# Performance work log

Hardware: AMD Instinct MI355X
Metric: run time of the kernel (lower is better)

Reference implementation:

```python
import jax, jax.numpy as jnp
import numpy as np

N, H, F, E, K = 2048, 1024, 4096, 8, 2


def setup_inputs() -> dict:
    key = jax.random.key(0)
    ks = jax.random.split(key, 6)
    x = jax.random.normal(ks[0], (N, H), dtype=jnp.float32)
    mapping = jax.random.randint(ks[1], (N, K), 0, E)
    Wg = jax.random.normal(ks[2], (E, H), dtype=jnp.float32) * (1.0 / np.sqrt(H))
    W1 = jax.random.normal(ks[3], (E, H, F), dtype=jnp.float32) * (1.0 / np.sqrt(H))
    b1 = jnp.zeros((E, F), dtype=jnp.float32)
    W2 = jax.random.normal(ks[4], (E, F, H), dtype=jnp.float32) * (1.0 / np.sqrt(F))
    b2 = jnp.zeros((E, H), dtype=jnp.float32)
    return {"x": x, "mapping": mapping, "Wg": Wg, "W1": W1, "b1": b1, "W2": W2, "b2": b2}


def reference(x, mapping, Wg, W1, b1, W2, b2):
    # Gate logits: note original applies softmax over dim=0 (the token axis).
    logits = jax.nn.softmax(x @ Wg.T, axis=0)  # [N, E]

    # Per-expert MLP. Original sorts tokens by expert, runs per-expert GEMMs on
    # dynamic splits, then unsorts -- mathematically: y[i,k] = MLP_{mapping[i,k]}(x[i]).
    # JIT-friendly dense baseline: run every expert over all tokens, gather per token.
    def mlp(e):
        h = jax.nn.gelu(x @ W1[e] + b1[e])  # [N, F]
        return h @ W2[e] + b2[e]            # [N, H]

    y_all = jnp.stack([mlp(e) for e in range(E)])  # [E, N, H]

    # Gate weights gathered per (token, k), normalized over top-k.
    w = jnp.take_along_axis(logits, mapping, axis=1)  # [N, K]
    w = w / jnp.sum(w, axis=-1, keepdims=True)

    idx = jnp.arange(x.shape[0])
    out = jnp.zeros_like(x)
    for k in range(mapping.shape[1]):
        yk = y_all[mapping[:, k], idx]  # [N, H] gather per token's k-th expert
        out = out + yk * w[:, k:k + 1]
    return out
```

## Files before the change

kernel.cpp:

```cpp
#include <hip/hip_runtime.h>

#define N_TOK 2048
#define HD    1024
#define FD    4096
#define NE    8

typedef __attribute__((ext_vector_type(8))) short short8;
typedef __attribute__((ext_vector_type(4))) float floatx4;

__device__ __forceinline__ unsigned short f2bf(float f) {
  unsigned int u = __float_as_uint(f);
  u += 0x7fffu + ((u >> 16) & 1u);
  return (unsigned short)(u >> 16);
}

__device__ __forceinline__ void gl2lds16(const unsigned short* g, unsigned short* l) {
  __builtin_amdgcn_global_load_lds(
      (const __attribute__((address_space(1))) unsigned int*)g,
      (__attribute__((address_space(3))) unsigned int*)l, 16, 0, 0);
}

__device__ __forceinline__ float gelu_tanh(float x) {
  float t = 0.7978845608028654f * x * (1.0f + 0.044715f * x * x);
  return 0.5f * x * (1.0f + tanhf(t));
}

__device__ __forceinline__ int poff_of(const int* __restrict__ cnt, int e) {
  int o = 0;
  for (int i = 0; i < e; ++i) o += (cnt[i] + 127) & ~127;
  return o;
}

__global__ void k_gating(const float* __restrict__ x, const float* __restrict__ wg,
                         float* __restrict__ p) {
  int wave = threadIdx.x >> 6;
  int lane = threadIdx.x & 63;
  int n = blockIdx.x * 4 + wave;
  const float4* xr = (const float4*)(x + (size_t)n * HD);
  float4 xv[4];
  #pragma unroll
  for (int i = 0; i < 4; ++i) xv[i] = xr[lane + i * 64];
  for (int e = 0; e < NE; ++e) {
    const float4* wr = (const float4*)(wg + (size_t)e * HD);
    float s = 0.f;
    #pragma unroll
    for (int i = 0; i < 4; ++i) {
      float4 w4 = wr[lane + i * 64];
      s += xv[i].x * w4.x + xv[i].y * w4.y + xv[i].z * w4.z + xv[i].w * w4.w;
    }
    for (int o = 32; o > 0; o >>= 1) s += __shfl_xor(s, o, 64);
    if (lane == 0) p[e * N_TOK + n] = s;
  }
}

__global__ void k_softmax(float* __restrict__ p) {
  int e = blockIdx.x;
  float* col = p + e * N_TOK;
  __shared__ float red[256];
  int t = threadIdx.x;
  float m = -1e30f;
  for (int i = t; i < N_TOK; i += 256) m = fmaxf(m, col[i]);
  red[t] = m; __syncthreads();
  for (int s = 128; s > 0; s >>= 1) { if (t < s) red[t] = fmaxf(red[t], red[t + s]); __syncthreads(); }
  m = red[0]; __syncthreads();
  float sum = 0.f;
  for (int i = t; i < N_TOK; i += 256) { float v = expf(col[i] - m); col[i] = v; sum += v; }
  red[t] = sum; __syncthreads();
  for (int s = 128; s > 0; s >>= 1) { if (t < s) red[t] += red[t + s]; __syncthreads(); }
  float inv = 1.0f / red[0];
  for (int i = t; i < N_TOK; i += 256) col[i] *= inv;
}

__global__ void k_route(const int* __restrict__ mp, const float* __restrict__ p,
                        int* __restrict__ cnt, int* __restrict__ idxl,
                        int* __restrict__ tke, int* __restrict__ tks, float* __restrict__ tkw) {
  int n = blockIdx.x * 256 + threadIdx.x;
  if (n >= N_TOK) return;
  int m0 = mp[n * 2 + 0], m1 = mp[n * 2 + 1];
  if (m0 == m1) {
    int s = atomicAdd(&cnt[m0], 1);
    idxl[m0 * N_TOK + s] = n;
    tke[n * 2] = m0; tks[n * 2] = s; tkw[n * 2] = 1.0f;
    tke[n * 2 + 1] = m0; tks[n * 2 + 1] = s; tkw[n * 2 + 1] = 0.0f;
  } else {
    float p0 = p[m0 * N_TOK + n], p1 = p[m1 * N_TOK + n];
    float inv = 1.0f / (p0 + p1);
    int s0 = atomicAdd(&cnt[m0], 1);
    idxl[m0 * N_TOK + s0] = n;
    tke[n * 2] = m0; tks[n * 2] = s0; tkw[n * 2] = p0 * inv;
    int s1 = atomicAdd(&cnt[m1], 1);
    idxl[m1 * N_TOK + s1] = n;
    tke[n * 2 + 1] = m1; tks[n * 2 + 1] = s1; tkw[n * 2 + 1] = p1 * inv;
  }
}

__global__ void k_gather(const float* __restrict__ x, const int* __restrict__ cnt,
                         const int* __restrict__ idxl, unsigned short* __restrict__ xg) {
  int e = blockIdx.y;
  int r = blockIdx.x;
  int c = cnt[e];
  int pc = (c + 127) & ~127;
  if (r >= pc) return;
  unsigned short* dst = xg + ((size_t)poff_of(cnt, e) + r) * HD;
  int t = threadIdx.x;
  union { unsigned short us[8]; uint4 v; } o;
  if (r < c) {
    const float* src = x + (size_t)idxl[e * N_TOK + r] * HD;
    float4 f0 = ((const float4*)src)[t * 2];
    float4 f1 = ((const float4*)src)[t * 2 + 1];
    o.us[0] = f2bf(f0.x); o.us[1] = f2bf(f0.y); o.us[2] = f2bf(f0.z); o.us[3] = f2bf(f0.w);
    o.us[4] = f2bf(f1.x); o.us[5] = f2bf(f1.y); o.us[6] = f2bf(f1.z); o.us[7] = f2bf(f1.w);
  } else {
    o.v.x = 0u; o.v.y = 0u; o.v.z = 0u; o.v.w = 0u;
  }
  ((uint4*)dst)[t] = o.v;
}

__global__ __launch_bounds__(256) void k_transcvt2(const float* __restrict__ w1,
                                                   unsigned short* __restrict__ w1t,
                                                   const float* __restrict__ w2,
                                                   unsigned short* __restrict__ w2t) {
  __shared__ float tile[64][65];
  int l = blockIdx.x;
  const float* src; unsigned short* dst; int rows, cols, bx, by, e;
  if (l < 8192) {
    src = w1; dst = w1t; rows = HD; cols = FD;
    bx = l & 63; by = (l >> 6) & 15; e = l >> 10;
  } else {
    int l2 = l - 8192;
    src = w2; dst = w2t; rows = FD; cols = HD;
    bx = l2 & 15; by = (l2 >> 4) & 63; e = l2 >> 10;
  }
  const size_t base = (size_t)e * rows * cols;
  int c0 = bx * 64, r0 = by * 64;
  int t = threadIdx.x;
  int lr = t >> 4;
  int lc = (t & 15) * 4;
  #pragma unroll
  for (int i = 0; i < 64; i += 16) {
    float4 v = *(const float4*)(src + base + (size_t)(r0 + lr + i) * cols + c0 + lc);
    tile[lr + i][lc] = v.x; tile[lr + i][lc + 1] = v.y;
    tile[lr + i][lc + 2] = v.z; tile[lr + i][lc + 3] = v.w;
  }
  __syncthreads();
  int oc = t >> 2;
  int rseg = (t & 3) * 16;
  union { unsigned short us[16]; uint4 v[2]; } o;
  #pragma unroll
  for (int i = 0; i < 16; ++i) o.us[i] = f2bf(tile[rseg + i][oc]);
  unsigned short* d = dst + base + (size_t)(c0 + oc) * rows + r0 + rseg;
  ((uint4*)d)[0] = o.v[0];
  ((uint4*)d)[1] = o.v[1];
}

__global__ __launch_bounds__(256) void k_gemm1(
    const unsigned short* __restrict__ xg, const unsigned short* __restrict__ w1t,
    const float* __restrict__ b1, const int* __restrict__ cnt,
    unsigned short* __restrict__ h) {
  const int l = blockIdx.x;
  const int r = l & 7;
  const int m = (l >> 3) & 31;
  const int q = l >> 8;
  const int e = q >> 2;
  const int n = ((q & 3) << 3) | r;

  const int c = cnt[e];
  const int mbase = m * 64;
  if (mbase >= c) return;
  const int nbase = n * 128;
  const int po = poff_of(cnt, e);
  const unsigned short* A = xg + ((size_t)po + mbase) * HD;
  const unsigned short* B = w1t + ((size_t)e * FD + nbase) * HD;

  __shared__ unsigned short As[64 * 32];
  __shared__ unsigned short Bs[128 * 32];

  const int tid = threadIdx.x;
  const int wave = tid >> 6, lane = tid & 63;
  const int quad = lane >> 4, lrow = lane & 15;
  const int wn = wave * 32;

  floatx4 acc[4][2];
  #pragma unroll
  for (int i = 0; i < 4; ++i)
    #pragma unroll
    for (int j = 0; j < 2; ++j) acc[i][j] = (floatx4){0.f, 0.f, 0.f, 0.f};

  const int rA = tid >> 2, kA = (((tid & 3) ^ ((tid >> 2) & 3)) & 3) * 8;
  const int rB0 = tid >> 2, kB0 = kA;
  const int rB1 = 64 + (tid >> 2), kB1 = kA;

  const int sx = lrow & 3;

  for (int kt = 0; kt < HD / 32; ++kt) {
    __syncthreads();
    const unsigned short* ga = A + kt * 32;
    const unsigned short* gb = B + kt * 32;
    gl2lds16(ga + (size_t)rA * HD + kA, As + (size_t)(wave * 64) * 8);
    gl2lds16(gb + (size_t)rB0 * HD + kB0, Bs + (size_t)(wave * 64) * 8);
    gl2lds16(gb + (size_t)rB1 * HD + kB1, Bs + (size_t)(256 + wave * 64) * 8);
    __syncthreads();
    short8 aF[4], bF[2];
    #pragma unroll
    for (int i = 0; i < 4; ++i)
      aF[i] = *(const short8*)(As + (i * 16 + lrow) * 32 + ((quad ^ sx) & 3) * 8);
    #pragma unroll
    for (int j = 0; j < 2; ++j)
      bF[j] = *(const short8*)(Bs + (wn + j * 16 + lrow) * 32 + ((quad ^ sx) & 3) * 8);
    #pragma unroll
    for (int i = 0; i < 4; ++i)
      #pragma unroll
      for (int j = 0; j < 2; ++j)
        acc[i][j] = __builtin_amdgcn_mfma_f32_16x16x32_bf16(aF[i], bF[j], acc[i][j], 0, 0, 0);
  }

  const size_t hrow0 = (size_t)po + mbase;
  #pragma unroll
  for (int i = 0; i < 4; ++i) {
    #pragma unroll
    for (int rr = 0; rr < 4; ++rr) {
      int row = i * 16 + quad * 4 + rr;
      unsigned short* hr = h + (hrow0 + row) * FD + nbase;
      #pragma unroll
      for (int j = 0; j < 2; ++j) {
        int col = wn + j * 16 + lrow;
        float v = acc[i][j][rr] + b1[e * FD + nbase + col];
        hr[col] = f2bf(gelu_tanh(v));
      }
    }
  }
}

__global__ __launch_bounds__(256) void k_gemm2(
    const unsigned short* __restrict__ h, const unsigned short* __restrict__ w2t,
    const int* __restrict__ cnt, unsigned short* __restrict__ ya) {
  const int l = blockIdx.x;
  const int nt = l & 15;
  const int mt = l >> 4;
  const int mbase = mt * 64;
  const int nbase = nt * 64;

  int e = -1, po = 0, ce = 0;
  {
    int o = 0;
    #pragma unroll
    for (int i = 0; i < NE; ++i) {
      int ci = cnt[i];
      int pc = (ci + 127) & ~127;
      if (mbase >= o && mbase < o + pc) { e = i; po = o; ce = ci; }
      o += pc;
    }
  }
  if (e < 0) return;
  if (mbase - po >= ce) return;

  const unsigned short* A = h + (size_t)mbase * FD;
  const unsigned short* B = w2t + ((size_t)e * HD + nbase) * FD;

  __shared__ unsigned short As[64 * 64];
  __shared__ unsigned short Bs[64 * 64];

  const int tid = threadIdx.x;
  const int wave = tid >> 6, lane = tid & 63;
  const int quad = lane >> 4, lrow = lane & 15;
  const int wm = (wave >> 1) * 32, wn = (wave & 1) * 32;

  floatx4 acc[2][2];
  #pragma unroll
  for (int i = 0; i < 2; ++i)
    #pragma unroll
    for (int j = 0; j < 2; ++j) acc[i][j] = (floatx4){0.f, 0.f, 0.f, 0.f};

  const int s0 = tid,       r0 = s0 >> 3, k0 = (((s0 & 7) ^ ((s0 >> 3) & 7)) & 7) * 8;
  const int s1 = 256 + tid, r1 = s1 >> 3, k1 = (((s1 & 7) ^ ((s1 >> 3) & 7)) & 7) * 8;

  const int sx8 = lrow & 7;

  for (int kt = 0; kt < FD / 64; ++kt) {
    __syncthreads();
    const unsigned short* ga = A + kt * 64;
    const unsigned short* gb = B + kt * 64;
    gl2lds16(ga + (size_t)r0 * FD + k0, As + (size_t)(wave * 64) * 8);
    gl2lds16(ga + (size_t)r1 * FD + k1, As + (size_t)(256 + wave * 64) * 8);
    gl2lds16(gb + (size_t)r0 * FD + k0, Bs + (size_t)(wave * 64) * 8);
    gl2lds16(gb + (size_t)r1 * FD + k1, Bs + (size_t)(256 + wave * 64) * 8);
    __syncthreads();
    #pragma unroll
    for (int c = 0; c < 2; ++c) {
      short8 aF[2], bF[2];
      #pragma unroll
      for (int i = 0; i < 2; ++i)
        aF[i] = *(const short8*)(As + (wm + i * 16 + lrow) * 64 + (((c * 4 + quad) ^ sx8) & 7) * 8);
      #pragma unroll
      for (int j = 0; j < 2; ++j)
        bF[j] = *(const short8*)(Bs + (wn + j * 16 + lrow) * 64 + (((c * 4 + quad) ^ sx8) & 7) * 8);
      #pragma unroll
      for (int i = 0; i < 2; ++i)
        #pragma unroll
        for (int j = 0; j < 2; ++j)
          acc[i][j] = __builtin_amdgcn_mfma_f32_16x16x32_bf16(aF[i], bF[j], acc[i][j], 0, 0, 0);
    }
  }

  #pragma unroll
  for (int i = 0; i < 2; ++i) {
    #pragma unroll
    for (int rr = 0; rr < 4; ++rr) {
      int row = mbase + wm + i * 16 + quad * 4 + rr;
      unsigned short* yr = ya + (size_t)row * HD + nbase;
      #pragma unroll
      for (int j = 0; j < 2; ++j) {
        int col = wn + j * 16 + lrow;
        yr[col] = f2bf(acc[i][j][rr]);
      }
    }
  }
}

__global__ __launch_bounds__(256) void k_combine(
    const unsigned short* __restrict__ ya, const float* __restrict__ b2,
    const int* __restrict__ cnt, const int* __restrict__ tke,
    const int* __restrict__ tks, const float* __restrict__ tkw,
    float* __restrict__ out) {
  int n = blockIdx.x;
  int e0 = tke[n * 2], e1 = tke[n * 2 + 1];
  int p0 = poff_of(cnt, e0) + tks[n * 2];
  int p1 = poff_of(cnt, e1) + tks[n * 2 + 1];
  float w0 = tkw[n * 2], w1 = tkw[n * 2 + 1];
  int c = threadIdx.x * 4;
  union { unsigned short us[4]; ushort2 u2[2]; unsigned long long ll; } y0, y1;
  y0.ll = *(const unsigned long long*)(ya + (size_t)p0 * HD + c);
  y1.ll = *(const unsigned long long*)(ya + (size_t)p1 * HD + c);
  float4 bb0 = *(const float4*)(b2 + (size_t)e0 * HD + c);
  float4 bb1 = *(const float4*)(b2 + (size_t)e1 * HD + c);
  float4 o;
  o.x = w0 * (__uint_as_float((unsigned)y0.us[0] << 16) + bb0.x) + w1 * (__uint_as_float((unsigned)y1.us[0] << 16) + bb1.x);
  o.y = w0 * (__uint_as_float((unsigned)y0.us[1] << 16) + bb0.y) + w1 * (__uint_as_float((unsigned)y1.us[1] << 16) + bb1.y);
  o.z = w0 * (__uint_as_float((unsigned)y0.us[2] << 16) + bb0.z) + w1 * (__uint_as_float((unsigned)y1.us[2] << 16) + bb1.z);
  o.w = w0 * (__uint_as_float((unsigned)y0.us[3] << 16) + bb0.w) + w1 * (__uint_as_float((unsigned)y1.us[3] << 16) + bb1.w);
  *(float4*)(out + (size_t)n * HD + c) = o;
}

extern "C" void kernel_launch(void* const* d_in, const int* in_sizes, int n_in,
                              void* d_out, int out_size, void* d_ws, size_t ws_size,
                              hipStream_t stream) {
  const float* x  = (const float*)d_in[0];
  const int*   mp = (const int*)d_in[1];
  const float* wg = (const float*)d_in[2];
  const float* w1 = (const float*)d_in[3];
  const float* b1 = (const float*)d_in[4];
  const float* w2 = (const float*)d_in[5];
  const float* b2 = (const float*)d_in[6];
  float* out = (float*)d_out;
  char* ws = (char*)d_ws;

  float* p    = (float*)(ws + 0);
  int*   cnt  = (int*)(ws + 65536);
  int*   idxl = (int*)(ws + 66048);
  int*   tke  = (int*)(ws + 131584);
  int*   tks  = (int*)(ws + 147968);
  float* tkw  = (float*)(ws + 164352);
  size_t off = 180736;
  unsigned short* w1t = (unsigned short*)(ws + off);  off += 67108864;
  unsigned short* w2t = (unsigned short*)(ws + off);  off += 67108864;
  unsigned short* xg  = (unsigned short*)(ws + off);  off += 10485760;
  unsigned short* h   = (unsigned short*)(ws + off);  off += 41943040;
  unsigned short* ya  = (unsigned short*)(ws + off);  off += 10485760;

  hipMemsetAsync(cnt, 0, 32, stream);

  k_gating<<<512, 256, 0, stream>>>(x, wg, p);
  k_softmax<<<NE, 256, 0, stream>>>(p);
  k_route<<<NE, 256, 0, stream>>>(mp, p, cnt, idxl, tke, tks, tkw);
  k_transcvt2<<<16384, 256, 0, stream>>>(w1, w1t, w2, w2t);
  k_gather<<<dim3(N_TOK, NE), 128, 0, stream>>>(x, cnt, idxl, xg);
  k_gemm1<<<8192, 256, 0, stream>>>(xg, w1t, b1, cnt, h);
  k_gemm2<<<80 * 16, 256, 0, stream>>>(h, w2t, cnt, ya);
  k_combine<<<N_TOK, 256, 0, stream>>>(ya, b2, cnt, tke, tks, tkw, out);
}
```

Before: 494.3 us.

## Pre-tile converted expert weights into contiguous 128x32 blocks for GEMM loads

```diff
diff --git a/kernel.cpp b/kernel.cpp
--- a/kernel.cpp
+++ b/kernel.cpp
@@ -116,41 +116,44 @@
   ((uint4*)dst)[t] = o.v;
 }
 
-__global__ __launch_bounds__(256) void k_transcvt2(const float* __restrict__ w1,
+__global__ __launch_bounds__(256) void k_transtile(const float* __restrict__ w1,
                                                    unsigned short* __restrict__ w1t,
                                                    const float* __restrict__ w2,
                                                    unsigned short* __restrict__ w2t) {
-  __shared__ float tile[64][65];
+  __shared__ float tile[32][129];
   int l = blockIdx.x;
-  const float* src; unsigned short* dst; int rows, cols, bx, by, e;
+  const float* src; unsigned short* dst; int ncols; size_t tbase;
+  int e, nt, kt;
   if (l < 8192) {
-    src = w1; dst = w1t; rows = HD; cols = FD;
-    bx = l & 63; by = (l >> 6) & 15; e = l >> 10;
+    e = l >> 10; nt = (l >> 5) & 31; kt = l & 31;
+    src = w1 + (size_t)e * HD * FD; ncols = FD;
+    dst = w1t; tbase = (((size_t)e * 32 + nt) * 32 + kt) * 4096;
   } else {
     int l2 = l - 8192;
-    src = w2; dst = w2t; rows = FD; cols = HD;
-    bx = l2 & 15; by = (l2 >> 4) & 63; e = l2 >> 10;
-  }
-  const size_t base = (size_t)e * rows * cols;
-  int c0 = bx * 64, r0 = by * 64;
-  int t = threadIdx.x;
-  int lr = t >> 4;
-  int lc = (t & 15) * 4;
-  #pragma unroll
-  for (int i = 0; i < 64; i += 16) {
-    float4 v = *(const float4*)(src + base + (size_t)(r0 + lr + i) * cols + c0 + lc);
-    tile[lr + i][lc] = v.x; tile[lr + i][lc + 1] = v.y;
-    tile[lr + i][lc + 2] = v.z; tile[lr + i][lc + 3] = v.w;
+    e = l2 >> 10; nt = (l2 >> 7) & 7; kt = l2 & 127;
+    src = w2 + (size_t)e * FD * HD; ncols = HD;
+    dst = w2t; tbase = (((size_t)e * 8 + nt) * 128 + kt) * 4096;
+  }
+  const int t = threadIdx.x;
+  const int c4 = t & 31;
+  const int rb = t >> 5;
+  #pragma unroll
+  for (int i = 0; i < 4; ++i) {
+    int r = rb + 8 * i;
+    float4 v = *(const float4*)(src + (size_t)(kt * 32 + r) * ncols + nt * 128 + c4 * 4);
+    tile[r][c4 * 4 + 0] = v.x; tile[r][c4 * 4 + 1] = v.y;
+    tile[r][c4 * 4 + 2] = v.z; tile[r][c4 * 4 + 3] = v.w;
   }
   __syncthreads();
-  int oc = t >> 2;
-  int rseg = (t & 3) * 16;
-  union { unsigned short us[16]; uint4 v[2]; } o;
-  #pragma unroll
-  for (int i = 0; i < 16; ++i) o.us[i] = f2bf(tile[rseg + i][oc]);
-  unsigned short* d = dst + base + (size_t)(c0 + oc) * rows + r0 + rseg;
-  ((uint4*)d)[0] = o.v[0];
-  ((uint4*)d)[1] = o.v[1];
+  #pragma unroll
+  for (int i = 0; i < 2; ++i) {
+    int o = t * 2 + i;
+    int n = o >> 2, kc = o & 3;
+    union { unsigned short us[8]; uint4 v; } u;
+    #pragma unroll
+    for (int j = 0; j < 8; ++j) u.us[j] = f2bf(tile[kc * 8 + j][n]);
+    *(uint4*)(dst + tbase + (size_t)o * 8) = u.v;
+  }
 }
 
 __global__ __launch_bounds__(256) void k_gemm1(
@@ -170,7 +173,7 @@
   const int nbase = n * 128;
   const int po = poff_of(cnt, e);
   const unsigned short* A = xg + ((size_t)po + mbase) * HD;
-  const unsigned short* B = w1t + ((size_t)e * FD + nbase) * HD;
+  const unsigned short* Bt = w1t + (((size_t)e * 32 + n) * 32) * 4096;
 
   __shared__ unsigned short As[64 * 32];
   __shared__ unsigned short Bs[128 * 32];
@@ -186,27 +189,22 @@
     #pragma unroll
     for (int j = 0; j < 2; ++j) acc[i][j] = (floatx4){0.f, 0.f, 0.f, 0.f};
 
-  const int rA = tid >> 2, kA = (((tid & 3) ^ ((tid >> 2) & 3)) & 3) * 8;
-  const int rB0 = tid >> 2, kB0 = kA;
-  const int rB1 = 64 + (tid >> 2), kB1 = kA;
-
-  const int sx = lrow & 3;
+  const int rA = tid >> 2, kA = (tid & 3) * 8;
 
   for (int kt = 0; kt < HD / 32; ++kt) {
     __syncthreads();
-    const unsigned short* ga = A + kt * 32;
-    const unsigned short* gb = B + kt * 32;
-    gl2lds16(ga + (size_t)rA * HD + kA, As + (size_t)(wave * 64) * 8);
-    gl2lds16(gb + (size_t)rB0 * HD + kB0, Bs + (size_t)(wave * 64) * 8);
-    gl2lds16(gb + (size_t)rB1 * HD + kB1, Bs + (size_t)(256 + wave * 64) * 8);
+    gl2lds16(A + kt * 32 + (size_t)rA * HD + kA, As + (size_t)wave * 512);
+    const unsigned short* gb = Bt + (size_t)kt * 4096 + (size_t)tid * 8;
+    gl2lds16(gb,        Bs + (size_t)wave * 512);
+    gl2lds16(gb + 2048, Bs + 2048 + (size_t)wave * 512);
     __syncthreads();
     short8 aF[4], bF[2];
     #pragma unroll
     for (int i = 0; i < 4; ++i)
-      aF[i] = *(const short8*)(As + (i * 16 + lrow) * 32 + ((quad ^ sx) & 3) * 8);
+      aF[i] = *(const short8*)(As + (i * 16 + lrow) * 32 + quad * 8);
     #pragma unroll
     for (int j = 0; j < 2; ++j)
-      bF[j] = *(const short8*)(Bs + (wn + j * 16 + lrow) * 32 + ((quad ^ sx) & 3) * 8);
+      bF[j] = *(const short8*)(Bs + (wn + j * 16 + lrow) * 32 + quad * 8);
     #pragma unroll
     for (int i = 0; i < 4; ++i)
       #pragma unroll
@@ -255,10 +253,11 @@
   if (mbase - po >= ce) return;
 
   const unsigned short* A = h + (size_t)mbase * FD;
-  const unsigned short* B = w2t + ((size_t)e * HD + nbase) * FD;
-
-  __shared__ unsigned short As[64 * 64];
-  __shared__ unsigned short Bs[64 * 64];
+  const unsigned short* Bt = w2t + (((size_t)e * 8 + (nt >> 1)) * 128) * 4096
+                                 + (size_t)(nt & 1) * 2048;
+
+  __shared__ unsigned short As[2 * 64 * 32];
+  __shared__ unsigned short Bs[2 * 64 * 32];
 
   const int tid = threadIdx.x;
   const int wave = tid >> 6, lane = tid & 63;
@@ -271,29 +270,27 @@
     #pragma unroll
     for (int j = 0; j < 2; ++j) acc[i][j] = (floatx4){0.f, 0.f, 0.f, 0.f};
 
-  const int s0 = tid,       r0 = s0 >> 3, k0 = (((s0 & 7) ^ ((s0 >> 3) & 7)) & 7) * 8;
-  const int s1 = 256 + tid, r1 = s1 >> 3, k1 = (((s1 & 7) ^ ((s1 >> 3) & 7)) & 7) * 8;
-
-  const int sx8 = lrow & 7;
+  const int r0 = tid >> 2, k0 = (tid & 3) * 8;
 
   for (int kt = 0; kt < FD / 64; ++kt) {
     __syncthreads();
-    const unsigned short* ga = A + kt * 64;
-    const unsigned short* gb = B + kt * 64;
-    gl2lds16(ga + (size_t)r0 * FD + k0, As + (size_t)(wave * 64) * 8);
-    gl2lds16(ga + (size_t)r1 * FD + k1, As + (size_t)(256 + wave * 64) * 8);
-    gl2lds16(gb + (size_t)r0 * FD + k0, Bs + (size_t)(wave * 64) * 8);
-    gl2lds16(gb + (size_t)r1 * FD + k1, Bs + (size_t)(256 + wave * 64) * 8);
+    #pragma unroll
+    for (int cc = 0; cc < 2; ++cc) {
+      gl2lds16(A + (size_t)r0 * FD + kt * 64 + cc * 32 + k0,
+               As + cc * 2048 + (size_t)wave * 512);
+      gl2lds16(Bt + (size_t)(kt * 2 + cc) * 4096 + (size_t)tid * 8,
+               Bs + cc * 2048 + (size_t)wave * 512);
+    }
     __syncthreads();
     #pragma unroll
-    for (int c = 0; c < 2; ++c) {
+    for (int cc = 0; cc < 2; ++cc) {
       short8 aF[2], bF[2];
       #pragma unroll
       for (int i = 0; i < 2; ++i)
-        aF[i] = *(const short8*)(As + (wm + i * 16 + lrow) * 64 + (((c * 4 + quad) ^ sx8) & 7) * 8);
+        aF[i] = *(const short8*)(As + cc * 2048 + (wm + i * 16 + lrow) * 32 + quad * 8);
       #pragma unroll
       for (int j = 0; j < 2; ++j)
-        bF[j] = *(const short8*)(Bs + (wn + j * 16 + lrow) * 64 + (((c * 4 + quad) ^ sx8) & 7) * 8);
+        bF[j] = *(const short8*)(Bs + cc * 2048 + (wn + j * 16 + lrow) * 32 + quad * 8);
       #pragma unroll
       for (int i = 0; i < 2; ++i)
         #pragma unroll
@@ -372,7 +369,7 @@
   k_gating<<<512, 256, 0, stream>>>(x, wg, p);
   k_softmax<<<NE, 256, 0, stream>>>(p);
   k_route<<<NE, 256, 0, stream>>>(mp, p, cnt, idxl, tke, tks, tkw);
-  k_transcvt2<<<16384, 256, 0, stream>>>(w1, w1t, w2, w2t);
+  k_transtile<<<16384, 256, 0, stream>>>(w1, w1t, w2, w2t);
   k_gather<<<dim3(N_TOK, NE), 128, 0, stream>>>(x, cnt, idxl, xg);
   k_gemm1<<<8192, 256, 0, stream>>>(xg, w1t, b1, cnt, h);
   k_gemm2<<<80 * 16, 256, 0, stream>>>(h, w2t, cnt, ya);
```

New measurement: 488.5 us. About the same (-1.2%).
